# Optimization experiments

Hardware: AMD Instinct MI355X
Metric: run time of the kernel (lower is better)

## Reference

```python
import math
import jax, jax.numpy as jnp
import numpy as np

E = 1024
H = 16
D = E // H  # 64

def _l2norm(t, eps=1e-12):
    n = jnp.sqrt(jnp.sum(t * t, axis=-1, keepdims=True))
    return t / jnp.maximum(n, eps)

def setup_inputs() -> dict:
    key = jax.random.key(0)
    ks = jax.random.split(key, 10)
    s = 0.02
    x = jax.random.normal(ks[0], (2, 4096, E), dtype=jnp.float32)
    Wq = jax.random.normal(ks[1], (E, E), dtype=jnp.float32) * s
    Wk = jax.random.normal(ks[2], (E, E), dtype=jnp.float32) * s
    Wv = jax.random.normal(ks[3], (E, E), dtype=jnp.float32) * s
    Walpha = jax.random.normal(ks[4], (E, H), dtype=jnp.float32) * s
    Wbeta = jax.random.normal(ks[5], (E, H), dtype=jnp.float32) * s
    A_log = jnp.linspace(0.0, math.log(16.0), H).astype(jnp.float32)
    dt_bias = jnp.zeros((H,), dtype=jnp.float32)
    Wgate = jax.random.normal(ks[6], (E, E), dtype=jnp.float32) * s
    Wout = jax.random.normal(ks[7], (E, E), dtype=jnp.float32) * s
    rms_w = jnp.ones((D,), dtype=jnp.float32)
    return {"x": x, "Wq": Wq, "Wk": Wk, "Wv": Wv, "Walpha": Walpha,
            "Wbeta": Wbeta, "A_log": A_log, "dt_bias": dt_bias,
            "Wgate": Wgate, "Wout": Wout, "rms_w": rms_w}

def reference(x, Wq, Wk, Wv, Walpha, Wbeta, A_log, dt_bias, Wgate, Wout, rms_w):
    b, s, _ = x.shape
    q = (x @ Wq).reshape(b, s, H, D)
    k = (x @ Wk).reshape(b, s, H, D)
    v = (x @ Wv).reshape(b, s, H, D)
    q = _l2norm(q) / math.sqrt(D)
    k = _l2norm(k)
    # gates: alpha in (0,1], beta in (0,1)   [b,s,H]
    dt = jax.nn.softplus(x @ Walpha + dt_bias)
    alpha = jnp.exp(-jnp.exp(A_log) * dt)
    beta = jax.nn.sigmoid(x @ Wbeta)

    # time-major for scan: [s,b,H,D] / [s,b,H]
    qT = jnp.moveaxis(q, 1, 0)
    kT = jnp.moveaxis(k, 1, 0)
    vT = jnp.moveaxis(v, 1, 0)
    aT = jnp.moveaxis(alpha, 1, 0)
    bT = jnp.moveaxis(beta, 1, 0)

    state0 = jnp.zeros((b, H, D, D), dtype=x.dtype)

    def step(state, inp):
        q_t, k_t, v_t, a_t, b_t = inp  # [b,H,D] x3, [b,H] x2
        state = a_t[..., None, None] * state
        stored = jnp.einsum('bhij,bhj->bhi', state, k_t)
        delta = b_t[..., None] * (v_t - stored)
        state = state + jnp.einsum('bhi,bhj->bhij', delta, k_t)
        o_t = jnp.einsum('bhij,bhj->bhi', state, q_t)
        return state, o_t

    # q,k,v are [s,b,H,D] -> per-step [b,H,D]
    qs = jnp.swapaxes(qT, 1, 2).swapaxes(1, 1)  # keep [s,b,H,D]
    _, outs = jax.lax.scan(step, state0, (qT, kT, vT, aT, bT))
    out = jnp.moveaxis(outs, 0, 1)  # [b,s,H,D]

    # RMSNorm over head_dim
    var = jnp.mean(out * out, axis=-1, keepdims=True)
    out = out * jax.lax.rsqrt(var + 1e-6) * rms_w

    out = out.reshape(b, s, E)
    gate = jax.nn.silu(x @ Wgate)
    return (out * gate) @ Wout
```

## Files before the change

kernel.cpp:

```cpp
#include <hip/hip_runtime.h>
#include <cstdint>
#include <cstddef>

typedef __bf16 bf16;
typedef __bf16 bf16x4 __attribute__((ext_vector_type(4)));
typedef __bf16 bf16x8 __attribute__((ext_vector_type(8)));
typedef float  f32x4  __attribute__((ext_vector_type(4)));

#define GLD_LDS16(gp, lp) \
  __builtin_amdgcn_global_load_lds((__attribute__((address_space(1))) void*)(gp), \
                                   (__attribute__((address_space(3))) void*)(lp), 16, 0, 0)

__device__ __forceinline__ f32x4 f32x4_zero(){ f32x4 v; v[0]=0.f; v[1]=0.f; v[2]=0.f; v[3]=0.f; return v; }

__device__ __forceinline__ f32x4 mfma16x16x32(bf16x8 a, bf16x8 b, f32x4 c){
  return __builtin_amdgcn_mfma_f32_16x16x32_bf16(a, b, c, 0, 0, 0);
}
__device__ __forceinline__ bf16x8 frag64(const bf16* base, int row0, int kk, int lane){
  return *(const bf16x8*)&base[(row0 + (lane&15))*64 + kk*32 + (lane>>4)*8];
}
__device__ __forceinline__ bf16x8 fragSwz(const bf16* base, int row0, int kk, int lane){
  const int row = row0 + (lane&15);
  const int off = (kk*32 + (lane>>4)*8) ^ ((row&7)<<3);
  return *(const bf16x8*)&base[row*64 + off];
}
struct bf2 { bf16 h, l; };
__device__ __forceinline__ bf2 split2(float v){
  bf2 r; r.h = (bf16)v; r.l = (bf16)(v - (float)r.h); return r;
}

__global__ __launch_bounds__(256) void k_cvt_x(const float* __restrict__ x,
                                               bf16* __restrict__ xh, bf16* __restrict__ xl, int n4){
  int i = blockIdx.x*256 + threadIdx.x;
  if (i < n4){
    float4 v = ((const float4*)x)[i];
    bf16x4 h, l;
    bf2 t0 = split2(v.x); h[0]=t0.h; l[0]=t0.l;
    bf2 t1 = split2(v.y); h[1]=t1.h; l[1]=t1.l;
    bf2 t2 = split2(v.z); h[2]=t2.h; l[2]=t2.l;
    bf2 t3 = split2(v.w); h[3]=t3.h; l[3]=t3.l;
    ((bf16x4*)xh)[i] = h;
    ((bf16x4*)xl)[i] = l;
  }
}

__global__ __launch_bounds__(256) void k_transpose_w(const float* __restrict__ W,
                                                     bf16* __restrict__ Wth, bf16* __restrict__ Wtl){
  __shared__ float tile[32][33];
  const int k0 = blockIdx.x*32, n0 = blockIdx.y*32;
  const int r = threadIdx.x >> 3, c4 = (threadIdx.x & 7)*4;
  float4 v = *(const float4*)&W[(size_t)(k0+r)*1024 + n0 + c4];
  tile[r][c4+0]=v.x; tile[r][c4+1]=v.y; tile[r][c4+2]=v.z; tile[r][c4+3]=v.w;
  __syncthreads();
  bf16x4 h, l;
  bf2 t0 = split2(tile[c4+0][r]); h[0]=t0.h; l[0]=t0.l;
  bf2 t1 = split2(tile[c4+1][r]); h[1]=t1.h; l[1]=t1.l;
  bf2 t2 = split2(tile[c4+2][r]); h[2]=t2.h; l[2]=t2.l;
  bf2 t3 = split2(tile[c4+3][r]); h[3]=t3.h; l[3]=t3.l;
  *(bf16x4*)&Wth[(size_t)(n0+r)*1024 + k0 + c4] = h;
  *(bf16x4*)&Wtl[(size_t)(n0+r)*1024 + k0 + c4] = l;
}

__global__ __launch_bounds__(256) void k_transpose_ab(const float* __restrict__ Wa, const float* __restrict__ Wb,
                                                      bf16* __restrict__ WabTh, bf16* __restrict__ WabTl){
  int p = blockIdx.x*256 + threadIdx.x;
  if (p < 32768){
    int o = p >> 10, k = p & 1023;
    float v = (o < 16) ? Wa[k*16 + o] : Wb[k*16 + (o-16)];
    bf2 s = split2(v);
    WabTh[p] = s.h;
    WabTl[p] = s.l;
  }
}

__global__ __launch_bounds__(256) void k_gemm3(const bf16* __restrict__ Ah, const bf16* __restrict__ Al,
                                               const bf16* __restrict__ Bth, const bf16* __restrict__ Btl,
                                               bf16* __restrict__ Cb, float* __restrict__ Cf){
  __shared__ bf16 Ash[128*32], Asl[128*32];
  __shared__ bf16 Bsh[128*32], Bsl[128*32];
  const int tid = threadIdx.x, lane = tid & 63, w = tid >> 6;
  const int wm = w >> 1, wn = w & 1;
  const size_t m0 = (size_t)blockIdx.x * 128;
  const size_t n0 = (size_t)blockIdx.y * 128;
  f32x4 acc[4][4];
  #pragma unroll
  for (int i=0;i<4;++i)
    #pragma unroll
    for (int j=0;j<4;++j) acc[i][j] = f32x4_zero();

  for (int k0 = 0; k0 < 1024; k0 += 32){
    __syncthreads();
    #pragma unroll
    for (int j = 0; j < 2; ++j){
      const int rbase = 32*w + 16*j;
      const int r = rbase + (lane >> 2);
      const int kk = k0 + (lane & 3)*8;
      GLD_LDS16(&Ah [(m0 + r)*1024 + kk], &Ash[rbase*32]);
      GLD_LDS16(&Al [(m0 + r)*1024 + kk], &Asl[rbase*32]);
      GLD_LDS16(&Bth[(n0 + r)*1024 + kk], &Bsh[rbase*32]);
      GLD_LDS16(&Btl[(n0 + r)*1024 + kk], &Bsl[rbase*32]);
    }
    __syncthreads();
    bf16x8 ah[4], al[4], bh[4], bl[4];
    #pragma unroll
    for (int t=0;t<4;++t){
      ah[t] = *(const bf16x8*)&Ash[(64*wm + 16*t + (lane&15))*32 + (lane>>4)*8];
      al[t] = *(const bf16x8*)&Asl[(64*wm + 16*t + (lane&15))*32 + (lane>>4)*8];
      bh[t] = *(const bf16x8*)&Bsh[(64*wn + 16*t + (lane&15))*32 + (lane>>4)*8];
      bl[t] = *(const bf16x8*)&Bsl[(64*wn + 16*t + (lane&15))*32 + (lane>>4)*8];
    }
    #pragma unroll
    for (int i=0;i<4;++i)
      #pragma unroll
      for (int j=0;j<4;++j){
        f32x4 t = acc[i][j];
        t = mfma16x16x32(ah[i], bh[j], t);
        t = mfma16x16x32(ah[i], bl[j], t);
        t = mfma16x16x32(al[i], bh[j], t);
        acc[i][j] = t;
      }
  }
  #pragma unroll
  for (int i=0;i<4;++i)
    #pragma unroll
    for (int j=0;j<4;++j)
      #pragma unroll
      for (int r=0;r<4;++r){
        size_t row = m0 + 64*wm + 16*i + (lane>>4)*4 + r;
        size_t col = n0 + 64*wn + 16*j + (lane&15);
        float v = acc[i][j][r];
        if (Cf) Cf[row*1024 + col] = v;
        else    Cb[row*1024 + col] = (bf16)v;
      }
}

__global__ __launch_bounds__(256) void k_gemm1(const bf16* __restrict__ Ah, const bf16* __restrict__ Bth,
                                               bf16* __restrict__ Cb, float* __restrict__ Cf){
  __shared__ bf16 Ash[128*32];
  __shared__ bf16 Bsh[128*32];
  const int tid = threadIdx.x, lane = tid & 63, w = tid >> 6;
  const int wm = w >> 1, wn = w & 1;
  const size_t m0 = (size_t)blockIdx.x * 128;
  const size_t n0 = (size_t)blockIdx.y * 128;
  f32x4 acc[4][4];
  #pragma unroll
  for (int i=0;i<4;++i)
    #pragma unroll
    for (int j=0;j<4;++j) acc[i][j] = f32x4_zero();

  for (int k0 = 0; k0 < 1024; k0 += 32){
    __syncthreads();
    #pragma unroll
    for (int j = 0; j < 2; ++j){
      const int rbase = 32*w + 16*j;
      const int r = rbase + (lane >> 2);
      const int kk = k0 + (lane & 3)*8;
      GLD_LDS16(&Ah [(m0 + r)*1024 + kk], &Ash[rbase*32]);
      GLD_LDS16(&Bth[(n0 + r)*1024 + kk], &Bsh[rbase*32]);
    }
    __syncthreads();
    bf16x8 ah[4], bh[4];
    #pragma unroll
    for (int t=0;t<4;++t){
      ah[t] = *(const bf16x8*)&Ash[(64*wm + 16*t + (lane&15))*32 + (lane>>4)*8];
      bh[t] = *(const bf16x8*)&Bsh[(64*wn + 16*t + (lane&15))*32 + (lane>>4)*8];
    }
    #pragma unroll
    for (int i=0;i<4;++i)
      #pragma unroll
      for (int j=0;j<4;++j)
        acc[i][j] = mfma16x16x32(ah[i], bh[j], acc[i][j]);
  }
  #pragma unroll
  for (int i=0;i<4;++i)
    #pragma unroll
    for (int j=0;j<4;++j)
      #pragma unroll
      for (int r=0;r<4;++r){
        size_t row = m0 + 64*wm + 16*i + (lane>>4)*4 + r;
        size_t col = n0 + 64*wn + 16*j + (lane&15);
        float v = acc[i][j][r];
        if (Cf) Cf[row*1024 + col] = v;
        else    Cb[row*1024 + col] = (bf16)v;
      }
}

__global__ __launch_bounds__(256) void k_ab_gemm(const bf16* __restrict__ xh, const bf16* __restrict__ xl,
    const bf16* __restrict__ WabTh, const bf16* __restrict__ WabTl,
    const float* __restrict__ A_log, const float* __restrict__ dt_bias,
    float* __restrict__ logA, float* __restrict__ betap){
  __shared__ bf16 Ash[2][2048], Asl[2][2048];
  const int tid = threadIdx.x, lane = tid & 63, w = tid >> 6;
  const int mt = w >> 1, nt = w & 1;
  const size_t m0 = (size_t)blockIdx.x * 32;
  const int srow = tid >> 3;
  const int scol = 8*((tid & 7) ^ (srow & 7));
  const size_t sg = (m0 + srow)*1024 + scol;

  f32x4 acc = f32x4_zero();
  GLD_LDS16(&xh[sg], &Ash[0][w*512]);
  GLD_LDS16(&xl[sg], &Asl[0][w*512]);
  for (int s = 0; s < 16; ++s){
    const int cur = s & 1;
    __syncthreads();
    if (s + 1 < 16){
      const size_t g = sg + (size_t)(s+1)*64;
      GLD_LDS16(&xh[g], &Ash[cur^1][w*512]);
      GLD_LDS16(&xl[g], &Asl[cur^1][w*512]);
    }
    const int k0 = s*64;
    #pragma unroll
    for (int kk = 0; kk < 2; ++kk){
      bf16x8 aH = fragSwz(Ash[cur], 16*mt, kk, lane);
      bf16x8 aL = fragSwz(Asl[cur], 16*mt, kk, lane);
      const size_t bo = (size_t)(16*nt + (lane&15))*1024 + k0 + kk*32 + (lane>>4)*8;
      bf16x8 bH = *(const bf16x8*)&WabTh[bo];
      bf16x8 bL = *(const bf16x8*)&WabTl[bo];
      acc = mfma16x16x32(aH, bH, acc);
      acc = mfma16x16x32(aH, bL, acc);
      acc = mfma16x16x32(aL, bH, acc);
    }
  }
  const int col = lane & 15;
  #pragma unroll
  for (int r = 0; r < 4; ++r){
    const size_t row = m0 + 16*mt + (lane>>4)*4 + r;
    float v = acc[r];
    if (nt == 0){
      float z = v + dt_bias[col];
      float dt = (z > 20.f) ? z : log1pf(expf(z));
      logA[row*16 + col] = -expf(A_log[col]) * dt;
    } else {
      betap[row*16 + col] = 1.f/(1.f + expf(-v));
    }
  }
}

__global__ __launch_bounds__(256) void k_norm_f32(float* __restrict__ qf, float* __restrict__ kf){
  const size_t p = (size_t)blockIdx.x*256 + threadIdx.x;
  {
    float4* q4 = (float4*)(qf + p*64);
    float4 v[16]; float s = 0.f;
    #pragma unroll
    for (int i=0;i<16;++i){ v[i]=q4[i]; s += v[i].x*v[i].x + v[i].y*v[i].y + v[i].z*v[i].z + v[i].w*v[i].w; }
    float sc = 0.125f / fmaxf(sqrtf(s), 1e-12f);
    #pragma unroll
    for (int i=0;i<16;++i){ v[i].x*=sc; v[i].y*=sc; v[i].z*=sc; v[i].w*=sc; q4[i]=v[i]; }
  }
  {
    float4* k4 = (float4*)(kf + p*64);
    float4 v[16]; float s = 0.f;
    #pragma unroll
    for (int i=0;i<16;++i){ v[i]=k4[i]; s += v[i].x*v[i].x + v[i].y*v[i].y + v[i].z*v[i].z + v[i].w*v[i].w; }
    float sc = 1.0f / fmaxf(sqrtf(s), 1e-12f);
    #pragma unroll
    for (int i=0;i<16;++i){ v[i].x*=sc; v[i].y*=sc; v[i].z*=sc; v[i].w*=sc; k4[i]=v[i]; }
  }
}

__global__ __launch_bounds__(256) void k_norm_b16(bf16* __restrict__ qb, bf16* __restrict__ kb){
  const size_t p = (size_t)blockIdx.x*256 + threadIdx.x;
  bf16* q = qb + p*64;
  bf16* k = kb + p*64;
  bf16x8 qv[8], kv[8];
  float sq = 0.f, sk = 0.f;
  #pragma unroll
  for (int i=0;i<8;++i){
    qv[i] = ((const bf16x8*)q)[i];
    kv[i] = ((const bf16x8*)k)[i];
    #pragma unroll
    for (int j=0;j<8;++j){ float a=(float)qv[i][j]; sq+=a*a; float b=(float)kv[i][j]; sk+=b*b; }
  }
  float scq = 0.125f / fmaxf(sqrtf(sq), 1e-12f);
  float sck = 1.0f   / fmaxf(sqrtf(sk), 1e-12f);
  #pragma unroll
  for (int i=0;i<8;++i){
    bf16x8 oq, ok;
    #pragma unroll
    for (int j=0;j<8;++j){ oq[j]=(bf16)((float)qv[i][j]*scq); ok[j]=(bf16)((float)kv[i][j]*sck); }
    ((bf16x8*)q)[i] = oq; ((bf16x8*)k)[i] = ok;
  }
}

__device__ __forceinline__ void load_split_tile(const float* f32, const bf16* b16,
                                                size_t tokbase, int h,
                                                bf16* Lh, bf16* Ll, int tid, int nthr){
  for (int i = tid; i < 1024; i += nthr){
    int t = i >> 4, c4 = (i & 15)*4;
    const size_t g = (tokbase + t)*1024 + (size_t)h*64 + c4;
    float4 v;
    if (f32) v = *(const float4*)&f32[g];
    else { bf16x4 b = *(const bf16x4*)&b16[g]; v.x=(float)b[0]; v.y=(float)b[1]; v.z=(float)b[2]; v.w=(float)b[3]; }
    bf16x4 hh, ll;
    bf2 s0 = split2(v.x); hh[0]=s0.h; ll[0]=s0.l;
    bf2 s1 = split2(v.y); hh[1]=s1.h; ll[1]=s1.l;
    bf2 s2 = split2(v.z); hh[2]=s2.h; ll[2]=s2.l;
    bf2 s3 = split2(v.w); hh[3]=s3.h; ll[3]=s3.l;
    const int off = c4 ^ ((t&7)<<3);
    *(bf16x4*)&Lh[t*64 + off] = hh;
    *(bf16x4*)&Ll[t*64 + off] = ll;
  }
}

__global__ __launch_bounds__(128) void k_phaseA(const float* __restrict__ kf32, const bf16* __restrict__ kb16,
    const float* __restrict__ vf, const float* __restrict__ logA, const float* __restrict__ betap,
    bf16* __restrict__ Wg, bf16* __restrict__ Dg, float* __restrict__ Pg, bf16* __restrict__ Bg){
  __shared__ bf16  Kh[64*64], Kl_[64*64];
  __shared__ float Ef[64*64];
  __shared__ bf16  KtT[64*64];
  bf16* DT = (bf16*)Ef;
  bf16* WT = ((bf16*)Ef) + 4096;
  const int tid = threadIdx.x, lane = tid & 63, wid = tid >> 6;
  const int c = blockIdx.x, h = blockIdx.y, b = blockIdx.z;
  const size_t tokbase = (size_t)b*4096 + (size_t)c*64;
  const size_t cbase = ((size_t)((b*16 + h)*64 + c)) * 4096;

  load_split_tile(kf32, kb16, tokbase, h, Kh, Kl_, tid, 128);
  const float bet = betap[(tokbase + lane)*16 + h];
  if (tid < 64){
    float la = logA[(tokbase + tid)*16 + h];
    #pragma unroll
    for (int dlt = 1; dlt < 64; dlt <<= 1){
      float o = __shfl_up(la, dlt);
      if (lane >= dlt) la += o;
    }
    Ef[tid] = la;
  }
  __syncthreads();

  #pragma unroll
  for (int tt = 0; tt < 2; ++tt){
    const int t0 = 32*wid + 16*tt;
    #pragma unroll
    for (int tu = 0; tu < 4; ++tu){
      f32x4 accm = f32x4_zero();
      #pragma unroll
      for (int kk = 0; kk < 2; ++kk){
        bf16x8 aH = fragSwz(Kh,  t0,    kk, lane);
        bf16x8 aL = fragSwz(Kl_, t0,    kk, lane);
        bf16x8 bH = fragSwz(Kh,  16*tu, kk, lane);
        bf16x8 bL = fragSwz(Kl_, 16*tu, kk, lane);
        accm = mfma16x16x32(aH, bH, accm);
        accm = mfma16x16x32(aH, bL, accm);
        accm = mfma16x16x32(aL, bH, accm);
      }
      #pragma unroll
      for (int r = 0; r < 4; ++r){
        int row = t0 + (lane>>4)*4 + r, col = 16*tu + (lane&15);
        float ev = (col < row) ? accm[r]*__expf(Ef[row] - Ef[col]) : 0.f;
        if (row > 0) Ef[row*64 + col] = ev;
      }
    }
  }
  {
    const float lgL = Ef[63];
    for (int i = tid; i < 4096; i += 128){
      int t = i & 63, j = i >> 6;
      int ks = j ^ ((t&7)<<3);
      float kv = (float)Kh[t*64 + ks] + (float)Kl_[t*64 + ks];
      KtT[j*64 + (t ^ ((j&7)<<3))] = (bf16)(__expf(lgL - Ef[t]) * kv);
    }
  }
  __syncthreads();

  const float gL = __expf(Ef[63]);

  {
    float Xv[64], d[64];
    if (wid == 0){
      #pragma unroll
      for (int t = 0; t < 64; ++t)
        Xv[t] = vf[(tokbase + t)*1024 + h*64 + lane];
    } else {
      #pragma unroll
      for (int t = 0; t < 64; ++t){
        int ks = lane ^ ((t&7)<<3);
        Xv[t] = __expf(Ef[t]) * ((float)Kh[t*64 + ks] + (float)Kl_[t*64 + ks]);
      }
    }
    #pragma unroll
    for (int bi = 0; bi < 4; ++bi){
      float pre[16];
      #pragma unroll
      for (int tt = 0; tt < 16; ++tt){
        const int t = 16*bi + tt;
        float a0=0.f,a1=0.f,a2=0.f,a3=0.f;
        #pragma unroll
        for (int r4 = 0; r4 < 4*bi; ++r4){
          float4 e = *(const float4*)&Ef[t*64 + r4*4];
          a0 += e.x * d[r4*4+0];
          a1 += e.y * d[r4*4+1];
          a2 += e.z * d[r4*4+2];
          a3 += e.w * d[r4*4+3];
        }
        pre[tt] = (a0+a1)+(a2+a3);
      }
      #pragma unroll
      for (int tt = 0; tt < 16; ++tt){
        const int t = 16*bi + tt;
        float s = pre[tt];
        #pragma unroll
        for (int j = 0; j < 16; ++j)
          if (j < tt) s += Ef[t*64 + 16*bi + j] * d[16*bi + j];
        d[t] = __shfl(bet, t) * (Xv[t] - s);
      }
    }
    __syncthreads();
    bf16* myT = wid ? WT : DT;
    #pragma unroll
    for (int s4 = 0; s4 < 16; ++s4){
      bf16x4 v4;
      v4[0]=(bf16)d[s4*4+0]; v4[1]=(bf16)d[s4*4+1];
      v4[2]=(bf16)d[s4*4+2]; v4[3]=(bf16)d[s4*4+3];
      *(bf16x4*)&myT[lane*64 + ((s4*4) ^ ((lane&7)<<3))] = v4;
    }
    bf16* myG = wid ? Wg : Dg;
    #pragma unroll
    for (int t = 0; t < 64; ++t)
      myG[cbase + (size_t)t*64 + lane] = (bf16)d[t];
  }
  __syncthreads();

  if (wid == 0){
    #pragma unroll
    for (int tj = 0; tj < 4; ++tj)
      #pragma unroll
      for (int ti = 0; ti < 4; ++ti){
        f32x4 acc = f32x4_zero();
        #pragma unroll
        for (int kk = 0; kk < 2; ++kk)
          acc = mfma16x16x32(fragSwz(KtT, 16*tj, kk, lane), fragSwz(WT, 16*ti, kk, lane), acc);
        #pragma unroll
        for (int r = 0; r < 4; ++r){
          int row = 16*tj + (lane>>4)*4 + r, col = 16*ti + (lane&15);
          Pg[cbase + (size_t)row*64 + col] = ((row == col) ? gL : 0.f) - acc[r];
        }
      }
  } else {
    #pragma unroll
    for (int ti = 0; ti < 4; ++ti)
      #pragma unroll
      for (int tj = 0; tj < 4; ++tj){
        f32x4 acc = f32x4_zero();
        #pragma unroll
        for (int kk = 0; kk < 2; ++kk)
          acc = mfma16x16x32(fragSwz(DT, 16*ti, kk, lane), fragSwz(KtT, 16*tj, kk, lane), acc);
        #pragma unroll
        for (int r = 0; r < 4; ++r){
          int row = 16*ti + (lane>>4)*4 + r, col = 16*tj + (lane&15);
          Bg[cbase + (size_t)row*64 + col] = (bf16)acc[r];
        }
      }
  }
}

__global__ __launch_bounds__(256) void k_phaseB1(const float* __restrict__ Pg, const bf16* __restrict__ Bg,
                                                 float* __restrict__ PsegT, float* __restrict__ BsegF){
  __shared__ bf16 PaccH[4096], PaccL[4096], BaccH[4096], BaccL[4096];
  __shared__ bf16 PcH[4096], PcL[4096];
  __shared__ bf16 BcS[4096];
  const int tid = threadIdx.x, lane = tid & 63, w = tid >> 6;
  const int seg = blockIdx.x;
  const size_t chain = blockIdx.y;
  f32x4 Pr[4], Br[4];
  #pragma unroll
  for (int it = 0; it < 4; ++it){
    #pragma unroll
    for (int r = 0; r < 4; ++r){
      int row = 16*w + (lane>>4)*4 + r, col = 16*it + (lane&15);
      Pr[it][r] = (row == col) ? 1.f : 0.f;
      Br[it][r] = 0.f;
    }
  }
  for (int i = 0; i < 8; ++i){
    const size_t cb = (chain*64 + (size_t)seg*8 + i)*4096;
    #pragma unroll
    for (int it = 0; it < 4; ++it)
      #pragma unroll
      for (int r = 0; r < 4; ++r){
        int row = 16*w + (lane>>4)*4 + r, col = 16*it + (lane&15);
        bf2 sp = split2(Pr[it][r]); PaccH[row*64+col] = sp.h; PaccL[row*64+col] = sp.l;
        bf2 sb = split2(Br[it][r]); BaccH[row*64+col] = sb.h; BaccL[row*64+col] = sb.l;
      }
    __syncthreads();
    for (int j = tid; j < 1024; j += 256){
      float4 pv = ((const float4*)(Pg + cb))[j];
      bf16x4 ph, pl;
      bf2 u0 = split2(pv.x); ph[0]=u0.h; pl[0]=u0.l;
      bf2 u1 = split2(pv.y); ph[1]=u1.h; pl[1]=u1.l;
      bf2 u2 = split2(pv.z); ph[2]=u2.h; pl[2]=u2.l;
      bf2 u3 = split2(pv.w); ph[3]=u3.h; pl[3]=u3.l;
      ((bf16x4*)PcH)[j] = ph; ((bf16x4*)PcL)[j] = pl;
    }
    for (int j = tid; j < 512; j += 256)
      ((uint4*)BcS)[j] = ((const uint4*)(Bg + cb))[j];
    __syncthreads();
    f32x4 nP[4], nB[4];
    #pragma unroll
    for (int it = 0; it < 4; ++it){ nP[it] = f32x4_zero(); nB[it] = f32x4_zero(); }
    #pragma unroll
    for (int kk = 0; kk < 2; ++kk){
      bf16x8 aPH = frag64(PaccH, 16*w, kk, lane), aPL = frag64(PaccL, 16*w, kk, lane);
      bf16x8 aBH = frag64(BaccH, 16*w, kk, lane), aBL = frag64(BaccL, 16*w, kk, lane);
      #pragma unroll
      for (int it = 0; it < 4; ++it){
        bf16x8 bH = frag64(PcH, 16*it, kk, lane), bL = frag64(PcL, 16*it, kk, lane);
        nP[it] = mfma16x16x32(aPH, bH, nP[it]);
        nP[it] = mfma16x16x32(aPH, bL, nP[it]);
        nP[it] = mfma16x16x32(aPL, bH, nP[it]);
        nB[it] = mfma16x16x32(aBH, bH, nB[it]);
        nB[it] = mfma16x16x32(aBH, bL, nB[it]);
        nB[it] = mfma16x16x32(aBL, bH, nB[it]);
      }
    }
    #pragma unroll
    for (int it = 0; it < 4; ++it)
      #pragma unroll
      for (int r = 0; r < 4; ++r){
        int row = 16*w + (lane>>4)*4 + r, col = 16*it + (lane&15);
        Pr[it][r] = nP[it][r];
        Br[it][r] = nB[it][r] + (float)BcS[row*64 + col];
      }
  }
  const size_t sb = (chain*8 + seg)*4096;
  #pragma unroll
  for (int it = 0; it < 4; ++it)
    #pragma unroll
    for (int r = 0; r < 4; ++r){
      int row = 16*w + (lane>>4)*4 + r, col = 16*it + (lane&15);
      PsegT[sb + (size_t)col*64 + row] = Pr[it][r];
      BsegF[sb + (size_t)row*64 + col] = Br[it][r];
    }
}

__global__ __launch_bounds__(256) void k_phaseB2(const float* __restrict__ PsegT, const float* __restrict__ BsegF,
                                                 float* __restrict__ S0g){
  __shared__ bf16 Sh[4096], Sl[4096], Ph[4096], Pl[4096];
  __shared__ float Bf[4096];
  const int tid = threadIdx.x, lane = tid & 63, w = tid >> 6;
  const size_t bid = blockIdx.x;
  f32x4 Sr[4];
  #pragma unroll
  for (int it = 0; it < 4; ++it) Sr[it] = f32x4_zero();
  for (int seg = 0; seg < 8; ++seg){
    const size_t sb  = (bid*8 + seg)*4096;
    const size_t s0b = (bid*64 + (size_t)seg*8)*4096;
    #pragma unroll
    for (int it = 0; it < 4; ++it)
      #pragma unroll
      for (int r = 0; r < 4; ++r){
        int row = 16*w + (lane>>4)*4 + r, col = 16*it + (lane&15);
        S0g[s0b + (size_t)row*64 + col] = Sr[it][r];
        bf2 sp = split2(Sr[it][r]); Sh[row*64+col] = sp.h; Sl[row*64+col] = sp.l;
      }
    __syncthreads();
    for (int j = tid; j < 1024; j += 256){
      float4 pv = ((const float4*)(PsegT + sb))[j];
      bf16x4 ph, pl;
      bf2 u0 = split2(pv.x); ph[0]=u0.h; pl[0]=u0.l;
      bf2 u1 = split2(pv.y); ph[1]=u1.h; pl[1]=u1.l;
      bf2 u2 = split2(pv.z); ph[2]=u2.h; pl[2]=u2.l;
      bf2 u3 = split2(pv.w); ph[3]=u3.h; pl[3]=u3.l;
      ((bf16x4*)Ph)[j] = ph; ((bf16x4*)Pl)[j] = pl;
      ((float4*)Bf)[j] = ((const float4*)(BsegF + sb))[j];
    }
    __syncthreads();
    f32x4 nS[4];
    #pragma unroll
    for (int it = 0; it < 4; ++it) nS[it] = f32x4_zero();
    #pragma unroll
    for (int kk = 0; kk < 2; ++kk){
      bf16x8 aH = frag64(Sh, 16*w, kk, lane), aL = frag64(Sl, 16*w, kk, lane);
      #pragma unroll
      for (int it = 0; it < 4; ++it){
        bf16x8 bH = frag64(Ph, 16*it, kk, lane), bL = frag64(Pl, 16*it, kk, lane);
        nS[it] = mfma16x16x32(aH, bH, nS[it]);
        nS[it] = mfma16x16x32(aH, bL, nS[it]);
        nS[it] = mfma16x16x32(aL, bH, nS[it]);
      }
    }
    #pragma unroll
    for (int it = 0; it < 4; ++it)
      #pragma unroll
      for (int r = 0; r < 4; ++r){
        int row = 16*w + (lane>>4)*4 + r, col = 16*it + (lane&15);
        Sr[it][r] = nS[it][r] + Bf[row*64 + col];
      }
  }
}

__global__ __launch_bounds__(256) void k_phaseB3(const float* __restrict__ Pg, const bf16* __restrict__ Bg,
                                                 float* __restrict__ S0g){
  __shared__ bf16 Sh[4096], Sl[4096], Ph[4096], Pl[4096];
  __shared__ bf16 BcS[4096];
  const int tid = threadIdx.x, lane = tid & 63, w = tid >> 6;
  const int seg = blockIdx.x;
  const size_t chain = blockIdx.y;
  const size_t segbase = chain*64 + (size_t)seg*8;
  f32x4 Sr[4];
  #pragma unroll
  for (int it = 0; it < 4; ++it)
    #pragma unroll
    for (int r = 0; r < 4; ++r){
      int row = 16*w + (lane>>4)*4 + r, col = 16*it + (lane&15);
      Sr[it][r] = S0g[segbase*4096 + (size_t)row*64 + col];
    }
  for (int i = 0; i < 7; ++i){
    const size_t cb = (segbase + i)*4096;
    #pragma unroll
    for (int it = 0; it < 4; ++it)
      #pragma unroll
      for (int r = 0; r < 4; ++r){
        int row = 16*w + (lane>>4)*4 + r, col = 16*it + (lane&15);
        bf2 sp = split2(Sr[it][r]); Sh[row*64+col] = sp.h; Sl[row*64+col] = sp.l;
      }
    __syncthreads();
    for (int j = tid; j < 1024; j += 256){
      float4 pv = ((const float4*)(Pg + cb))[j];
      bf16x4 ph, pl;
      bf2 u0 = split2(pv.x); ph[0]=u0.h; pl[0]=u0.l;
      bf2 u1 = split2(pv.y); ph[1]=u1.h; pl[1]=u1.l;
      bf2 u2 = split2(pv.z); ph[2]=u2.h; pl[2]=u2.l;
      bf2 u3 = split2(pv.w); ph[3]=u3.h; pl[3]=u3.l;
      ((bf16x4*)Ph)[j] = ph; ((bf16x4*)Pl)[j] = pl;
    }
    for (int j = tid; j < 512; j += 256)
      ((uint4*)BcS)[j] = ((const uint4*)(Bg + cb))[j];
    __syncthreads();
    f32x4 nS[4];
    #pragma unroll
    for (int it = 0; it < 4; ++it) nS[it] = f32x4_zero();
    #pragma unroll
    for (int kk = 0; kk < 2; ++kk){
      bf16x8 aH = frag64(Sh, 16*w, kk, lane), aL = frag64(Sl, 16*w, kk, lane);
      #pragma unroll
      for (int it = 0; it < 4; ++it){
        bf16x8 bH = frag64(Ph, 16*it, kk, lane), bL = frag64(Pl, 16*it, kk, lane);
        nS[it] = mfma16x16x32(aH, bH, nS[it]);
        nS[it] = mfma16x16x32(aH, bL, nS[it]);
        nS[it] = mfma16x16x32(aL, bH, nS[it]);
      }
    }
    const size_t outb = (segbase + i + 1)*4096;
    #pragma unroll
    for (int it = 0; it < 4; ++it)
      #pragma unroll
      for (int r = 0; r < 4; ++r){
        int row = 16*w + (lane>>4)*4 + r, col = 16*it + (lane&15);
        float v = nS[it][r] + (float)BcS[row*64 + col];
        Sr[it][r] = v;
        S0g[outb + (size_t)row*64 + col] = v;
      }
  }
}

__global__ __launch_bounds__(256, 2) void k_phaseC(
    const float* __restrict__ qf32, const bf16* __restrict__ qb16,
    const float* __restrict__ kf32, const bf16* __restrict__ kb16,
    const bf16* __restrict__ gf, const float* __restrict__ logA,
    const float* __restrict__ S0g, const bf16* __restrict__ Wg, const bf16* __restrict__ Dg,
    const float* __restrict__ rms_w, bf16* __restrict__ yh, bf16* __restrict__ yl){
  __shared__ bf16 Qh[4096], Ql[4096], Kh[4096], Klo[4096];
  __shared__ bf16 Wl_[4096], Dl_[4096];
  __shared__ bf16 S0h[4096], S0l[4096];
  __shared__ bf16 AAg[4096];
  __shared__ bf16 BDt[4096];
  const int tid = threadIdx.x, lane = tid & 63, w = tid >> 6;
  const int c = blockIdx.x, h = blockIdx.y, b = blockIdx.z;
  const size_t tokbase = (size_t)b*4096 + (size_t)c*64;
  const size_t cbase = ((size_t)((b*16 + h)*64 + c)) * 4096;

  load_split_tile(qf32, qb16, tokbase, h, Qh, Ql, tid, 256);
  load_split_tile(kf32, kb16, tokbase, h, Kh, Klo, tid, 256);
  for (int i = tid; i < 512; i += 256){
    int r = i >> 3, d = r*8 + ((i&7) ^ (r&7));
    ((uint4*)Wl_)[d] = ((const uint4*)(Wg + cbase))[i];
    ((uint4*)Dl_)[d] = ((const uint4*)(Dg + cbase))[i];
  }
  for (int i = tid; i < 1024; i += 256){
    float4 v = ((const float4*)(S0g + cbase))[i];
    bf16x4 sh, sl;
    bf2 t0 = split2(v.x); sh[0]=t0.h; sl[0]=t0.l;
    bf2 t1 = split2(v.y); sh[1]=t1.h; sl[1]=t1.l;
    bf2 t2 = split2(v.z); sh[2]=t2.h; sl[2]=t2.l;
    bf2 t3 = split2(v.w); sh[3]=t3.h; sl[3]=t3.l;
    int t = i >> 4, off = ((i&15)*4) ^ ((t&7)<<3);
    *(bf16x4*)&S0h[t*64 + off] = sh;
    *(bf16x4*)&S0l[t*64 + off] = sl;
  }
  float la = logA[(tokbase + lane)*16 + h];
  #pragma unroll
  for (int dlt = 1; dlt < 64; dlt <<= 1){
    float o = __shfl_up(la, dlt);
    if (lane >= dlt) la += o;
  }
  __syncthreads();

  {
    const int t0 = 16*w;
    #pragma unroll
    for (int tu = 0; tu < 4; ++tu){
      f32x4 accm = f32x4_zero();
      #pragma unroll
      for (int kk = 0; kk < 2; ++kk){
        bf16x8 aH = fragSwz(Qh,  t0,    kk, lane);
        bf16x8 aL = fragSwz(Ql,  t0,    kk, lane);
        bf16x8 bH = fragSwz(Kh,  16*tu, kk, lane);
        bf16x8 bL = fragSwz(Klo, 16*tu, kk, lane);
        accm = mfma16x16x32(aH, bH, accm);
        accm = mfma16x16x32(aH, bL, accm);
        accm = mfma16x16x32(aL, bH, accm);
      }
      #pragma unroll
      for (int r = 0; r < 4; ++r){
        int row = t0 + (lane>>4)*4 + r, col = 16*tu + (lane&15);
        float lgr = __shfl(la, row), lgc = __shfl(la, col);
        float v = (col <= row) ? accm[r]*__expf(lgr - lgc) : 0.f;
        AAg[row*64 + (col ^ ((row&7)<<3))] = (bf16)v;
      }
    }
  }
  {
    const int i0 = 16*w;
    #pragma unroll
    for (int tu = 0; tu < 4; ++tu){
      f32x4 accm = f32x4_zero();
      #pragma unroll
      for (int kk = 0; kk < 2; ++kk){
        bf16x8 aH = fragSwz(S0h, i0,    kk, lane);
        bf16x8 aL = fragSwz(S0l, i0,    kk, lane);
        bf16x8 bb = fragSwz(Wl_, 16*tu, kk, lane);
        accm = mfma16x16x32(aH, bb, accm);
        accm = mfma16x16x32(aL, bb, accm);
      }
      #pragma unroll
      for (int r = 0; r < 4; ++r){
        int row = i0 + (lane>>4)*4 + r, col = 16*tu + (lane&15);
        float v = (float)Dl_[col*64 + (row ^ ((col&7)<<3))] - accm[r];
        BDt[row*64 + (col ^ ((row&7)<<3))] = (bf16)v;
      }
    }
  }
  __syncthreads();
  for (int i = tid; i < 4096; i += 256){
    int t = i >> 6;
    float gq = __expf(__shfl(la, t));
    float v = gq * ((float)Qh[i] + (float)Ql[i]);
    bf2 sp = split2(v);
    Qh[i] = sp.h; Ql[i] = sp.l;
  }
  __syncthreads();
  {
    const int t0 = 16*w;
    f32x4 o_acc[4];
    #pragma unroll
    for (int it = 0; it < 4; ++it) o_acc[it] = f32x4_zero();
    #pragma unroll
    for (int kk = 0; kk < 2; ++kk){
      bf16x8 aQh = fragSwz(Qh, t0, kk, lane);
      bf16x8 aQl = fragSwz(Ql, t0, kk, lane);
      bf16x8 aA  = fragSwz(AAg, t0, kk, lane);
      #pragma unroll
      for (int it = 0; it < 4; ++it){
        bf16x8 bSh = fragSwz(S0h, 16*it, kk, lane);
        bf16x8 bSl = fragSwz(S0l, 16*it, kk, lane);
        bf16x8 bD  = fragSwz(BDt, 16*it, kk, lane);
        f32x4 t = o_acc[it];
        t = mfma16x16x32(aQh, bSh, t);
        t = mfma16x16x32(aQh, bSl, t);
        t = mfma16x16x32(aQl, bSh, t);
        t = mfma16x16x32(aA,  bD,  t);
        o_acc[it] = t;
      }
    }
    float rw[4];
    #pragma unroll
    for (int it = 0; it < 4; ++it) rw[it] = rms_w[16*it + (lane&15)];
    #pragma unroll
    for (int r = 0; r < 4; ++r){
      float ss = 0.f;
      #pragma unroll
      for (int it = 0; it < 4; ++it) ss += o_acc[it][r]*o_acc[it][r];
      ss += __shfl_xor(ss, 1); ss += __shfl_xor(ss, 2);
      ss += __shfl_xor(ss, 4); ss += __shfl_xor(ss, 8);
      const float scale = rsqrtf(ss*(1.f/64.f) + 1e-6f);
      const int row = t0 + (lane>>4)*4 + r;
      const size_t tok = tokbase + row;
      #pragma unroll
      for (int it = 0; it < 4; ++it){
        const int col = 16*it + (lane&15);
        float g = (float)gf[tok*1024 + h*64 + col];
        float sg = g / (1.f + __expf(-g));
        float v = o_acc[it][r]*scale*rw[it]*sg;
        bf2 sp = split2(v);
        yh[tok*1024 + h*64 + col] = sp.h;
        yl[tok*1024 + h*64 + col] = sp.l;
      }
    }
  }
}

extern "C" void kernel_launch(void* const* d_in, const int* in_sizes, int n_in,
                              void* d_out, int out_size, void* d_ws, size_t ws_size,
                              hipStream_t stream){
  const float* x     = (const float*)d_in[0];
  const float* Wq    = (const float*)d_in[1];
  const float* Wk    = (const float*)d_in[2];
  const float* Wv    = (const float*)d_in[3];
  const float* Wa    = (const float*)d_in[4];
  const float* Wb    = (const float*)d_in[5];
  const float* A_log = (const float*)d_in[6];
  const float* dt_b  = (const float*)d_in[7];
  const float* Wgt   = (const float*)d_in[8];
  const float* Wo    = (const float*)d_in[9];
  const float* rms_w = (const float*)d_in[10];

  const bool BIG = ws_size >= (size_t)215000000;

  char* ws = (char*)d_ws;
  size_t off = 0;
  auto alloc = [&](size_t bytes)->char*{
    char* p = ws + off;
    off += (bytes + 255) & ~(size_t)255;
    return p;
  };
  const size_t PLANE = (size_t)8192*1024*2;
  const size_t WPL   = (size_t)1024*1024*2;
  bf16* xh  = (bf16*)alloc(PLANE);
  bf16* xl  = (bf16*)alloc(PLANE);
  bf16* wqh = (bf16*)alloc(WPL); bf16* wql = (bf16*)alloc(WPL);
  bf16* wkh = (bf16*)alloc(WPL); bf16* wkl = (bf16*)alloc(WPL);
  bf16* wvh = (bf16*)alloc(WPL); bf16* wvl = (bf16*)alloc(WPL);
  bf16* wgh = (bf16*)alloc(WPL); bf16* wgl = (bf16*)alloc(WPL);
  bf16* woh = (bf16*)alloc(WPL); bf16* wol = (bf16*)alloc(WPL);
  bf16* WabTh = (bf16*)alloc((size_t)32*1024*2);
  bf16* WabTl = (bf16*)alloc((size_t)32*1024*2);
  float* qf = nullptr; bf16* qb = nullptr;
  float* kf = nullptr; bf16* kb = nullptr;
  if (BIG){ qf = (float*)alloc((size_t)8192*1024*4); kf = (float*)alloc((size_t)8192*1024*4); }
  else    { qb = (bf16*) alloc(PLANE);               kb = (bf16*) alloc(PLANE); }
  float* vf  = (float*)alloc((size_t)8192*1024*4);
  bf16* gfb  = (bf16*)alloc(PLANE);
  float* logA  = (float*)alloc((size_t)8192*16*4);
  float* betap = (float*)alloc((size_t)8192*16*4);
  bf16* Wg  = (bf16*)alloc((size_t)2048*4096*2);
  bf16* Dg  = (bf16*)alloc((size_t)2048*4096*2);
  float* Pg  = (float*)xh;
  float* S0g = vf;
  bf16* Bg   = wqh;
  float* PsegT = (float*)d_out;
  float* BsegF = (float*)d_out + 1048576;
  bf16* yh = xh;
  bf16* yl = xl;

  k_cvt_x<<<8192, 256, 0, stream>>>(x, xh, xl, 2097152);
  k_transpose_w<<<dim3(32,32), 256, 0, stream>>>(Wq,  wqh, wql);
  k_transpose_w<<<dim3(32,32), 256, 0, stream>>>(Wk,  wkh, wkl);
  k_transpose_w<<<dim3(32,32), 256, 0, stream>>>(Wv,  wvh, wvl);
  k_transpose_w<<<dim3(32,32), 256, 0, stream>>>(Wgt, wgh, wgl);
  k_transpose_w<<<dim3(32,32), 256, 0, stream>>>(Wo,  woh, wol);
  k_transpose_ab<<<128, 256, 0, stream>>>(Wa, Wb, WabTh, WabTl);

  if (BIG){
    k_gemm1<<<dim3(64,8), 256, 0, stream>>>(xh, wqh, nullptr, qf);
    k_gemm1<<<dim3(64,8), 256, 0, stream>>>(xh, wkh, nullptr, kf);
  } else {
    k_gemm1<<<dim3(64,8), 256, 0, stream>>>(xh, wqh, qb, nullptr);
    k_gemm1<<<dim3(64,8), 256, 0, stream>>>(xh, wkh, kb, nullptr);
  }
  k_gemm1<<<dim3(64,8), 256, 0, stream>>>(xh, wvh, nullptr, vf);
  k_gemm1<<<dim3(64,8), 256, 0, stream>>>(xh, wgh, gfb, nullptr);

  k_ab_gemm<<<256, 256, 0, stream>>>(xh, xl, WabTh, WabTl, A_log, dt_b, logA, betap);
  if (BIG) k_norm_f32<<<512, 256, 0, stream>>>(qf, kf);
  else     k_norm_b16<<<512, 256, 0, stream>>>(qb, kb);

  k_phaseA<<<dim3(64,16,2), 128, 0, stream>>>(kf, kb, vf, logA, betap, Wg, Dg, Pg, Bg);
  k_phaseB1<<<dim3(8,32), 256, 0, stream>>>(Pg, Bg, PsegT, BsegF);
  k_phaseB2<<<32, 256, 0, stream>>>(PsegT, BsegF, S0g);
  k_phaseB3<<<dim3(8,32), 256, 0, stream>>>(Pg, Bg, S0g);
  k_phaseC<<<dim3(64,16,2), 256, 0, stream>>>(qf, qb, kf, kb, gfb, logA, S0g, Wg, Dg, rms_w, yh, yl);

  k_gemm3<<<dim3(64,8), 256, 0, stream>>>(yh, yl, woh, wol, nullptr, (float*)d_out);
}
```

Baseline: 594.2 us.

## Fuse q/k L2 norm into GEMM epilogue and shrink phaseA shared memory

The per-head L2 normalisation of q and k moves into the k_gemm1 epilogue. Each wave's 64-column slice is exactly one head, so a 16-lane shuffle reduction gives the norm, which removes the separate norm kernel and its extra read/write pass over q and k. k_phaseA is also restructured: the intra-chunk triangular solve now uses a right-looking block update with in-place d, dropping the Xv and pre register arrays. The transposed-K buffer is built after the solve, aliasing existing LDS, which cuts shared memory so launch_bounds(128,4) can allow higher occupancy. The risk is a heavier GEMM epilogue and a different ordering of floating-point accumulation in the solve.

```diff
diff --git a/kernel.cpp b/kernel.cpp
--- a/kernel.cpp
+++ b/kernel.cpp
@@ -134,6 +134,7 @@
       }
 }
 
+template<int NRM>
 __global__ __launch_bounds__(256) void k_gemm1(const bf16* __restrict__ Ah, const bf16* __restrict__ Bth,
                                                bf16* __restrict__ Cb, float* __restrict__ Cf){
   __shared__ bf16 Ash[128*32];
@@ -174,15 +175,25 @@
   #pragma unroll
   for (int i=0;i<4;++i)
     #pragma unroll
-    for (int j=0;j<4;++j)
-      #pragma unroll
-      for (int r=0;r<4;++r){
+    for (int r=0;r<4;++r){
+      float sc = 1.f;
+      if (NRM){
+        float ss = 0.f;
+        #pragma unroll
+        for (int j=0;j<4;++j) ss += acc[i][j][r]*acc[i][j][r];
+        ss += __shfl_xor(ss, 1); ss += __shfl_xor(ss, 2);
+        ss += __shfl_xor(ss, 4); ss += __shfl_xor(ss, 8);
+        sc = (NRM==1 ? 0.125f : 1.0f) / fmaxf(sqrtf(ss), 1e-12f);
+      }
+      #pragma unroll
+      for (int j=0;j<4;++j){
         size_t row = m0 + 64*wm + 16*i + (lane>>4)*4 + r;
         size_t col = n0 + 64*wn + 16*j + (lane&15);
-        float v = acc[i][j][r];
+        float v = acc[i][j][r]*sc;
         if (Cf) Cf[row*1024 + col] = v;
         else    Cb[row*1024 + col] = (bf16)v;
       }
+    }
 }
 
 __global__ __launch_bounds__(256) void k_ab_gemm(const bf16* __restrict__ xh, const bf16* __restrict__ xl,
@@ -233,52 +244,6 @@
     } else {
       betap[row*16 + col] = 1.f/(1.f + expf(-v));
     }
-  }
-}
-
-__global__ __launch_bounds__(256) void k_norm_f32(float* __restrict__ qf, float* __restrict__ kf){
-  const size_t p = (size_t)blockIdx.x*256 + threadIdx.x;
-  {
-    float4* q4 = (float4*)(qf + p*64);
-    float4 v[16]; float s = 0.f;
-    #pragma unroll
-    for (int i=0;i<16;++i){ v[i]=q4[i]; s += v[i].x*v[i].x + v[i].y*v[i].y + v[i].z*v[i].z + v[i].w*v[i].w; }
-    float sc = 0.125f / fmaxf(sqrtf(s), 1e-12f);
-    #pragma unroll
-    for (int i=0;i<16;++i){ v[i].x*=sc; v[i].y*=sc; v[i].z*=sc; v[i].w*=sc; q4[i]=v[i]; }
-  }
-  {
-    float4* k4 = (float4*)(kf + p*64);
-    float4 v[16]; float s = 0.f;
-    #pragma unroll
-    for (int i=0;i<16;++i){ v[i]=k4[i]; s += v[i].x*v[i].x + v[i].y*v[i].y + v[i].z*v[i].z + v[i].w*v[i].w; }
-    float sc = 1.0f / fmaxf(sqrtf(s), 1e-12f);
-    #pragma unroll
-    for (int i=0;i<16;++i){ v[i].x*=sc; v[i].y*=sc; v[i].z*=sc; v[i].w*=sc; k4[i]=v[i]; }
-  }
-}
-
-__global__ __launch_bounds__(256) void k_norm_b16(bf16* __restrict__ qb, bf16* __restrict__ kb){
-  const size_t p = (size_t)blockIdx.x*256 + threadIdx.x;
-  bf16* q = qb + p*64;
-  bf16* k = kb + p*64;
-  bf16x8 qv[8], kv[8];
-  float sq = 0.f, sk = 0.f;
-  #pragma unroll
-  for (int i=0;i<8;++i){
-    qv[i] = ((const bf16x8*)q)[i];
-    kv[i] = ((const bf16x8*)k)[i];
-    #pragma unroll
-    for (int j=0;j<8;++j){ float a=(float)qv[i][j]; sq+=a*a; float b=(float)kv[i][j]; sk+=b*b; }
-  }
-  float scq = 0.125f / fmaxf(sqrtf(sq), 1e-12f);
-  float sck = 1.0f   / fmaxf(sqrtf(sk), 1e-12f);
-  #pragma unroll
-  for (int i=0;i<8;++i){
-    bf16x8 oq, ok;
-    #pragma unroll
-    for (int j=0;j<8;++j){ oq[j]=(bf16)((float)qv[i][j]*scq); ok[j]=(bf16)((float)kv[i][j]*sck); }
-    ((bf16x8*)q)[i] = oq; ((bf16x8*)k)[i] = ok;
   }
 }
 
@@ -302,14 +267,14 @@
   }
 }
 
-__global__ __launch_bounds__(128) void k_phaseA(const float* __restrict__ kf32, const bf16* __restrict__ kb16,
+__global__ __launch_bounds__(128, 4) void k_phaseA(const float* __restrict__ kf32, const bf16* __restrict__ kb16,
     const float* __restrict__ vf, const float* __restrict__ logA, const float* __restrict__ betap,
     bf16* __restrict__ Wg, bf16* __restrict__ Dg, float* __restrict__ Pg, bf16* __restrict__ Bg){
-  __shared__ bf16  Kh[64*64], Kl_[64*64];
-  __shared__ float Ef[64*64];
-  __shared__ bf16  KtT[64*64];
-  bf16* DT = (bf16*)Ef;
-  bf16* WT = ((bf16*)Ef) + 4096;
+  __shared__ bf16  Kh[4096], Kl_[4096];
+  __shared__ float Ef[4096];
+  bf16* DT  = Kh;
+  bf16* WT  = Kl_;
+  bf16* KtT = (bf16*)&Ef[2048];
   const int tid = threadIdx.x, lane = tid & 63, wid = tid >> 6;
   const int c = blockIdx.x, h = blockIdx.y, b = blockIdx.z;
   const size_t tokbase = (size_t)b*4096 + (size_t)c*64;
@@ -352,60 +317,65 @@
       }
     }
   }
+  __syncthreads();
+
+  float d[64];
   {
-    const float lgL = Ef[63];
-    for (int i = tid; i < 4096; i += 128){
-      int t = i & 63, j = i >> 6;
-      int ks = j ^ ((t&7)<<3);
-      float kv = (float)Kh[t*64 + ks] + (float)Kl_[t*64 + ks];
-      KtT[j*64 + (t ^ ((j&7)<<3))] = (bf16)(__expf(lgL - Ef[t]) * kv);
-    }
-  }
-  __syncthreads();
-
-  const float gL = __expf(Ef[63]);
-
-  {
-    float Xv[64], d[64];
     if (wid == 0){
       #pragma unroll
       for (int t = 0; t < 64; ++t)
-        Xv[t] = vf[(tokbase + t)*1024 + h*64 + lane];
+        d[t] = vf[(tokbase + t)*1024 + h*64 + lane];
     } else {
       #pragma unroll
       for (int t = 0; t < 64; ++t){
         int ks = lane ^ ((t&7)<<3);
-        Xv[t] = __expf(Ef[t]) * ((float)Kh[t*64 + ks] + (float)Kl_[t*64 + ks]);
+        d[t] = __expf(Ef[t]) * ((float)Kh[t*64 + ks] + (float)Kl_[t*64 + ks]);
       }
     }
     #pragma unroll
     for (int bi = 0; bi < 4; ++bi){
-      float pre[16];
       #pragma unroll
       for (int tt = 0; tt < 16; ++tt){
         const int t = 16*bi + tt;
-        float a0=0.f,a1=0.f,a2=0.f,a3=0.f;
-        #pragma unroll
-        for (int r4 = 0; r4 < 4*bi; ++r4){
-          float4 e = *(const float4*)&Ef[t*64 + r4*4];
-          a0 += e.x * d[r4*4+0];
-          a1 += e.y * d[r4*4+1];
-          a2 += e.z * d[r4*4+2];
-          a3 += e.w * d[r4*4+3];
-        }
-        pre[tt] = (a0+a1)+(a2+a3);
-      }
-      #pragma unroll
-      for (int tt = 0; tt < 16; ++tt){
-        const int t = 16*bi + tt;
-        float s = pre[tt];
+        float s = 0.f;
         #pragma unroll
         for (int j = 0; j < 16; ++j)
           if (j < tt) s += Ef[t*64 + 16*bi + j] * d[16*bi + j];
-        d[t] = __shfl(bet, t) * (Xv[t] - s);
-      }
-    }
-    __syncthreads();
+        d[t] = __shfl(bet, t) * (d[t] - s);
+      }
+      #pragma unroll
+      for (int b2 = bi + 1; b2 < 4; ++b2)
+        #pragma unroll
+        for (int tt = 0; tt < 16; ++tt){
+          const int t = 16*b2 + tt;
+          float a0=0.f,a1=0.f,a2=0.f,a3=0.f;
+          #pragma unroll
+          for (int q = 0; q < 4; ++q){
+            float4 e = *(const float4*)&Ef[t*64 + 16*bi + q*4];
+            a0 += e.x * d[16*bi + q*4 + 0];
+            a1 += e.y * d[16*bi + q*4 + 1];
+            a2 += e.z * d[16*bi + q*4 + 2];
+            a3 += e.w * d[16*bi + q*4 + 3];
+          }
+          d[t] -= (a0+a1)+(a2+a3);
+        }
+    }
+  }
+  __syncthreads();
+
+  {
+    const float gsc = __expf(Ef[63] - Ef[lane]);
+    for (int i = tid; i < 4096; i += 128){
+      int t = lane, j = i >> 6;
+      int ks = j ^ ((t&7)<<3);
+      float kv = (float)Kh[t*64 + ks] + (float)Kl_[t*64 + ks];
+      KtT[j*64 + (t ^ ((j&7)<<3))] = (bf16)(gsc * kv);
+    }
+  }
+  __syncthreads();
+
+  const float gL = __expf(Ef[63]);
+  {
     bf16* myT = wid ? WT : DT;
     #pragma unroll
     for (int s4 = 0; s4 < 16; ++s4){
@@ -862,18 +832,16 @@
   k_transpose_ab<<<128, 256, 0, stream>>>(Wa, Wb, WabTh, WabTl);
 
   if (BIG){
-    k_gemm1<<<dim3(64,8), 256, 0, stream>>>(xh, wqh, nullptr, qf);
-    k_gemm1<<<dim3(64,8), 256, 0, stream>>>(xh, wkh, nullptr, kf);
+    k_gemm1<1><<<dim3(64,8), 256, 0, stream>>>(xh, wqh, nullptr, qf);
+    k_gemm1<2><<<dim3(64,8), 256, 0, stream>>>(xh, wkh, nullptr, kf);
   } else {
-    k_gemm1<<<dim3(64,8), 256, 0, stream>>>(xh, wqh, qb, nullptr);
-    k_gemm1<<<dim3(64,8), 256, 0, stream>>>(xh, wkh, kb, nullptr);
-  }
-  k_gemm1<<<dim3(64,8), 256, 0, stream>>>(xh, wvh, nullptr, vf);
-  k_gemm1<<<dim3(64,8), 256, 0, stream>>>(xh, wgh, gfb, nullptr);
+    k_gemm1<1><<<dim3(64,8), 256, 0, stream>>>(xh, wqh, qb, nullptr);
+    k_gemm1<2><<<dim3(64,8), 256, 0, stream>>>(xh, wkh, kb, nullptr);
+  }
+  k_gemm1<0><<<dim3(64,8), 256, 0, stream>>>(xh, wvh, nullptr, vf);
+  k_gemm1<0><<<dim3(64,8), 256, 0, stream>>>(xh, wgh, gfb, nullptr);
 
   k_ab_gemm<<<256, 256, 0, stream>>>(xh, xl, WabTh, WabTl, A_log, dt_b, logA, betap);
-  if (BIG) k_norm_f32<<<512, 256, 0, stream>>>(qf, kf);
-  else     k_norm_b16<<<512, 256, 0, stream>>>(qb, kb);
 
   k_phaseA<<<dim3(64,16,2), 128, 0, stream>>>(kf, kb, vf, logA, betap, Wg, Dg, Pg, Bg);
   k_phaseB1<<<dim3(8,32), 256, 0, stream>>>(Pg, Bg, PsegT, BsegF);
```

New measurement: 513.9 us. 1.16x faster.
